# Optimization experiments

Measured on AMD Instinct MI355X. Metric: run time of the kernel, lower is better.

The kernel has to match this reference:

```python
import jax, jax.numpy as jnp
import numpy as np
import math


def setup_inputs() -> dict:
    key = jax.random.key(0)
    ks = jax.random.split(key, 4)
    B, C, H, W, D = 16, 512, 64, 64, 256
    return {
        "x": jax.random.normal(ks[0], (B, C, H, W), jnp.float32),
        "weight_global": jax.random.normal(ks[1], (C, D), jnp.float32) * 0.02,  # trunc_normal std=0.02
        "conv_g_w": jax.random.normal(ks[2], (C, C), jnp.float32) * 0.02,       # 1x1 conv, no bias
        "bn_g_gamma": jnp.ones((C,), jnp.float32),
        "bn_g_beta": jnp.zeros((C,), jnp.float32),
        "conv_c_w": jax.random.normal(ks[3], (C, C), jnp.float32) * 0.02,
        "bn_c_gamma": jnp.ones((C,), jnp.float32),
        "bn_c_beta": jnp.zeros((C,), jnp.float32),
    }


def _bn(x, gamma, beta, eps=1e-5):
    # BatchNorm2d in default training mode: batch statistics over (B, H, W)
    mean = x.mean(axis=(0, 2, 3), keepdims=True)
    var = x.var(axis=(0, 2, 3), keepdims=True)
    xn = (x - mean) * jax.lax.rsqrt(var + eps)
    return xn * gamma[None, :, None, None] + beta[None, :, None, None]


def reference(x, weight_global, conv_g_w, bn_g_gamma, bn_g_beta, conv_c_w, bn_c_gamma, bn_c_beta):
    b, c, h, w = x.shape
    inv_sqrt_c = 1.0 / math.sqrt(c)

    # Description: QR-orthogonal codebook, Q: (c, d)
    Q, _ = jnp.linalg.qr(weight_global + 1e-8)

    # global branch: 1x1 conv -> BN -> ReLU -> global avg pool
    gx = jnp.einsum('oc,bchw->bohw', conv_g_w, x)
    gx = jax.nn.relu(_bn(gx, bn_g_gamma, bn_g_beta))
    g = gx.mean(axis=(2, 3))                                  # (b, c)
    aff_g = jax.nn.softmax((g @ Q) * inv_sqrt_c, axis=1)      # (b, d)
    g = jax.nn.sigmoid(aff_g @ Q.T)                           # (b, c)

    # channel branch: 1x1 conv -> BN -> ReLU
    cx = jnp.einsum('oc,bchw->bohw', conv_c_w, x)
    cx = jax.nn.relu(_bn(cx, bn_c_gamma, bn_c_beta))
    ch = cx.reshape(b, c, h * w).transpose(0, 2, 1)           # (b, hw, c)
    aff_c = jax.nn.softmax((ch @ Q) * inv_sqrt_c, axis=2)     # (b, hw, d)
    # sum(diag_embed(aff_c) @ Q.T, dim=2) == aff_c @ Q.T (fused, avoids (b,hw,d,c) intermediate)
    ch = aff_c @ Q.T                                          # (b, hw, c)

    o = ch * g[:, None, :]
    o = o.transpose(0, 2, 1).reshape(b, c, h, w)
    return o + x
```

## Files before the change

### kernel.cpp

```cpp
#include <hip/hip_runtime.h>
#include <hip/hip_bf16.h>

#define BB 16
#define CC 512
#define HWP 4096
#define DD 256
#define NPIX 65536
#define INV_SQRT_C 0.04419417382415922f

typedef unsigned short u16;
typedef __attribute__((ext_vector_type(8))) short s16x8;
typedef __attribute__((ext_vector_type(8))) unsigned short u16x8;
typedef __attribute__((ext_vector_type(4))) unsigned short u16x4;
typedef __attribute__((ext_vector_type(4))) float f32x4;

__device__ __forceinline__ u16 f2b(float f){
  unsigned int u = __builtin_bit_cast(unsigned int, f);
  unsigned int r = (u + 0x7fffu + ((u >> 16) & 1u)) >> 16;
  return (u16)r;
}

__device__ __forceinline__ f32x4 mfma16(s16x8 a, s16x8 b, f32x4 c){
  return __builtin_amdgcn_mfma_f32_16x16x32_bf16(a, b, c, 0, 0, 0);
}

__global__ __launch_bounds__(512) void k_gram(const float* __restrict__ x, float* __restrict__ Spart,
                                              float* __restrict__ xbar, int kspl){
  __shared__ __align__(16) u16 Asl[128*72];
  __shared__ __align__(16) u16 Bsl[128*72];
  int tid = threadIdx.x;
  int w = tid >> 6, lane = tid & 63, lr = lane & 15, g = lane >> 4;
  int b = blockIdx.y;
  int kz = blockIdx.z;
  int t = blockIdx.x, ti = 0, rem = 4;
  while (t >= rem){ t -= rem; ++ti; --rem; }
  int tj = ti + t;
  int r0 = ti*128, c0 = tj*128;
  bool isdiag = (ti == tj);
  int wm = w >> 2, wn = w & 3;
  f32x4 acc[4][2] = {};
  float xsum[8] = {};
  const float* xb = x + (size_t)b*CC*HWP;
  int klen = HWP / kspl;
  int kbase = kz * klen;
  for (int k0 = kbase; k0 < kbase + klen; k0 += 64){
    __syncthreads();
    #pragma unroll
    for (int s = 0; s < 8; ++s){
      int tt = tid + s*512;
      int arr = tt >> 11;
      int row = (tt >> 4) & 127;
      int q = tt & 15;
      const float* src = xb + (size_t)((arr ? c0 : r0) + row)*HWP + k0 + q*4;
      f32x4 v = *(const f32x4*)src;
      if (isdiag && arr == 0) xsum[s] += (v[0]+v[1]) + (v[2]+v[3]);
      u16x4 u; u[0]=f2b(v[0]); u[1]=f2b(v[1]); u[2]=f2b(v[2]); u[3]=f2b(v[3]);
      u16* dst = (arr ? Bsl : Asl) + row*72 + q*4;
      *(u16x4*)dst = u;
    }
    __syncthreads();
    #pragma unroll
    for (int kc = 0; kc < 2; ++kc){
      s16x8 av[4], bv[2];
      #pragma unroll
      for (int mt = 0; mt < 4; ++mt) av[mt] = *(const s16x8*)&Asl[(wm*64 + mt*16 + lr)*72 + kc*32 + g*8];
      #pragma unroll
      for (int nt = 0; nt < 2; ++nt) bv[nt] = *(const s16x8*)&Bsl[(wn*32 + nt*16 + lr)*72 + kc*32 + g*8];
      #pragma unroll
      for (int mt = 0; mt < 4; ++mt)
        #pragma unroll
        for (int nt = 0; nt < 2; ++nt)
          acc[mt][nt] = mfma16(av[mt], bv[nt], acc[mt][nt]);
    }
  }
  float* sp = Spart + (size_t)(b*kspl + kz)*262144;
  #pragma unroll
  for (int mt = 0; mt < 4; ++mt)
    #pragma unroll
    for (int nt = 0; nt < 2; ++nt)
      #pragma unroll
      for (int r = 0; r < 4; ++r)
        sp[(size_t)(r0 + wm*64 + mt*16 + 4*g + r)*512 + c0 + wn*32 + nt*16 + lr] = acc[mt][nt][r];

  if (isdiag){
    __syncthreads();
    float* scr = (float*)Asl;
    #pragma unroll
    for (int s = 0; s < 8; ++s){
      int tt = tid + s*512;
      if ((tt >> 11) == 0){
        int row = (tt >> 4) & 127, q = tt & 15;
        scr[row*16 + q] = xsum[s];
      }
    }
    __syncthreads();
    if (tid < 128){
      float rs = 0.f;
      #pragma unroll
      for (int j = 0; j < 16; ++j) rs += scr[tid*16 + j];
      atomicAdd(&xbar[r0 + tid], rs * (1.0f/(float)NPIX));
    }
  }
}

__global__ __launch_bounds__(256) void k_sreduce(const float* __restrict__ Spart, float* __restrict__ S, int nslots){
  int idx = blockIdx.x*256 + threadIdx.x;
  int i = idx >> 9, j = idx & 511;
  int src = ((i >> 7) <= (j >> 7)) ? idx : (j*512 + i);
  float s = 0.f;
  for (int k = 0; k < nslots; ++k) s += Spart[(size_t)k*262144 + src];
  S[idx] = s;
}

__global__ __launch_bounds__(256) void k_G(const float* __restrict__ wg, float* __restrict__ G){
  int i = blockIdx.x, j = threadIdx.x;
  float s = 0.f;
  for (int c = 0; c < CC; ++c)
    s = fmaf(wg[c*DD + i] + 1e-8f, wg[c*DD + j] + 1e-8f, s);
  G[i*DD + j] = s;
}

__global__ __launch_bounds__(256) void k_cholPanel(float* __restrict__ G, int kb){
  int tid = threadIdx.x;
  int lane = tid & 63;
  int j = lane & 31;
  int K0 = kb*32;
  float c[32];
  #pragma unroll
  for (int i = 0; i < 32; ++i)
    c[i] = (i <= j) ? G[(K0+i)*DD + K0 + j] : 0.f;
  #pragma unroll
  for (int k = 0; k < 32; ++k){
    float piv = __shfl(c[k], k);
    float sd = sqrtf(piv);
    float ukj = c[k] / sd;
    c[k] = ukj;
    float uk[32];
    #pragma unroll
    for (int i = k + 1; i < 32; ++i) uk[i] = __shfl(ukj, i);
    #pragma unroll
    for (int i = k + 1; i < 32; ++i) c[i] -= uk[i] * ukj;
  }
  if (tid < 32){
    #pragma unroll
    for (int i = 0; i < 32; ++i)
      if (i <= j) G[(K0+i)*DD + K0 + j] = c[i];
  }
  int nt = 256 - K0 - 32;
  int jg = K0 + 32 + tid;
  if (tid < nt){
    float y[32];
    #pragma unroll
    for (int i = 0; i < 32; ++i) y[i] = G[(K0+i)*DD + jg];
    #pragma unroll
    for (int i = 0; i < 32; ++i){
      float s0 = y[i];
      #pragma unroll
      for (int l = 0; l < 32; ++l)
        if (l < i) s0 -= __shfl(c[l], i) * y[l];
      y[i] = s0 / __shfl(c[i], i);
    }
    #pragma unroll
    for (int i = 0; i < 32; ++i) G[(K0+i)*DD + jg] = y[i];
  }
}

__global__ __launch_bounds__(256) void k_cholTrail(float* __restrict__ G, int kb){
  int K0 = kb*32;
  int nt = 256 - K0 - 32;
  int T = (nt + 63) >> 6;
  int t = blockIdx.x, ti = 0, rem = T;
  while (t >= rem){ t -= rem; ++ti; --rem; }
  int tj = ti + t;
  int r0 = K0 + 32 + ti*64;
  int c0 = K0 + 32 + tj*64;
  __shared__ __align__(16) float Ur[32][64];
  __shared__ __align__(16) float Uc[32][64];
  int tid = threadIdx.x;
  for (int idx = tid; idx < 2048; idx += 256){
    int k = idx >> 6, cc = idx & 63;
    int gr = r0 + cc, gc = c0 + cc;
    Ur[k][cc] = (gr < 256) ? G[(K0+k)*DD + gr] : 0.f;
    Uc[k][cc] = (gc < 256) ? G[(K0+k)*DD + gc] : 0.f;
  }
  __syncthreads();
  int tr = (tid >> 4) * 4;
  int tc = (tid & 15) * 4;
  float acc[4][4] = {};
  #pragma unroll
  for (int k = 0; k < 32; ++k){
    f32x4 a = *(const f32x4*)&Ur[k][tr];
    f32x4 b = *(const f32x4*)&Uc[k][tc];
    #pragma unroll
    for (int ii = 0; ii < 4; ++ii)
      #pragma unroll
      for (int jj = 0; jj < 4; ++jj)
        acc[ii][jj] += a[ii]*b[jj];
  }
  #pragma unroll
  for (int ii = 0; ii < 4; ++ii){
    int gi = r0 + tr + ii;
    if (gi >= 256) continue;
    #pragma unroll
    for (int jj = 0; jj < 4; ++jj){
      int gj = c0 + tc + jj;
      if (gj < 256 && gj >= gi)
        G[gi*DD + gj] -= acc[ii][jj];
    }
  }
}

__global__ __launch_bounds__(256) void k_qsolve(const float* __restrict__ G,
    const float* __restrict__ wg,
    float* __restrict__ Q, float* __restrict__ Qst,
    u16* __restrict__ Qb, u16* __restrict__ Qstb){
  __shared__ __align__(16) float Pp[8192];
  __shared__ float Qlds[256*64];
  __shared__ float Wred[3*32*64];
  int tid = threadIdx.x;
  int w = tid >> 6, lane = tid & 63;
  int c = blockIdx.x*64 + lane;
  const float* arow = wg + (size_t)c*DD;

  for (int J = 0; J < 8; ++J){
    int J0 = J*32;
    int nrows8 = (J0 + 32)*8;
    for (int idx = tid; idx < nrows8; idx += 256){
      int row = idx >> 3, q = idx & 7;
      *(f32x4*)&Pp[row*32 + q*4] = *(const f32x4*)&G[row*256 + J0 + q*4];
    }
    __syncthreads();

    float W[32];
    if (w == 0){
      #pragma unroll
      for (int r = 0; r < 32; ++r) W[r] = arow[J0 + r] + 1e-8f;
    } else {
      #pragma unroll
      for (int r = 0; r < 32; ++r) W[r] = 0.f;
    }
    for (int M = w; M < J; M += 4){
      #pragma unroll 4
      for (int k = 0; k < 32; ++k){
        int row = M*32 + k;
        float qv = Qlds[row*64 + lane];
        const float* pr = &Pp[row*32];
        #pragma unroll
        for (int r4 = 0; r4 < 8; ++r4){
          f32x4 p = *(const f32x4*)&pr[r4*4];
          W[r4*4+0] -= qv*p[0];
          W[r4*4+1] -= qv*p[1];
          W[r4*4+2] -= qv*p[2];
          W[r4*4+3] -= qv*p[3];
        }
      }
    }
    if (w > 0){
      #pragma unroll
      for (int r = 0; r < 32; ++r) Wred[((w-1)*32 + r)*64 + lane] = W[r];
    }
    __syncthreads();

    if (w == 0){
      #pragma unroll
      for (int r = 0; r < 32; ++r)
        W[r] += Wred[r*64 + lane] + Wred[(32+r)*64 + lane] + Wred[(64+r)*64 + lane];
      #pragma unroll
      for (int i = 0; i < 32; ++i){
        float t = W[i];
        for (int l = 0; l < i; ++l) t -= W[l] * Pp[(J0 + l)*32 + i];
        W[i] = t / Pp[(J0 + i)*32 + i];
      }
      #pragma unroll
      for (int i = 0; i < 32; ++i) Qlds[(J0 + i)*64 + lane] = W[i];
      #pragma unroll
      for (int r4 = 0; r4 < 8; ++r4){
        f32x4 q4; u16x4 qb4;
        #pragma unroll
        for (int jj = 0; jj < 4; ++jj){ q4[jj] = W[r4*4+jj]; qb4[jj] = f2b(W[r4*4+jj]); }
        *(f32x4*)&Q[(size_t)c*DD + J0 + r4*4] = q4;
        *(u16x4*)&Qb[(size_t)c*DD + J0 + r4*4] = qb4;
      }
      #pragma unroll
      for (int i = 0; i < 32; ++i){
        float qs = W[i] * INV_SQRT_C;
        Qst[(size_t)(J0 + i)*CC + c] = qs;
        Qstb[(size_t)(J0 + i)*CC + c] = f2b(qs);
      }
    }
    __syncthreads();
  }
}

__global__ __launch_bounds__(256) void k_fold(const float* __restrict__ Wg, const float* __restrict__ Wc,
    const float* __restrict__ gamg, const float* __restrict__ betg,
    const float* __restrict__ gamc, const float* __restrict__ betc,
    const float* __restrict__ S, const float* __restrict__ xbar,
    float* __restrict__ Wgf, float* __restrict__ bgf,
    float* __restrict__ Wcf, float* __restrict__ bcf,
    u16* __restrict__ Wgb, u16* __restrict__ Wcb){
  int o = blockIdx.x & 511, br = blockIdx.x >> 9;
  int tid = threadIdx.x;
  int wv = tid >> 6, lane = tid & 63;
  const float* W = br ? Wc : Wg;
  __shared__ float wrow[512];
  __shared__ float red[256];
  __shared__ float yred[4];
  __shared__ float sc_s, bi_s;
  wrow[tid] = W[o*512 + tid]; wrow[tid+256] = W[o*512 + tid + 256];
  __syncthreads();

  float qp = 0.f;
  for (int c1 = wv; c1 < 512; c1 += 4){
    const float* srow = S + (size_t)c1*512;
    float y = 0.f;
    #pragma unroll
    for (int c8 = 0; c8 < 8; ++c8){
      int c2 = lane + c8*64;
      y = fmaf(srow[c2], wrow[c2], y);
    }
    y += __shfl_xor(y, 1);
    y += __shfl_xor(y, 2);
    y += __shfl_xor(y, 4);
    y += __shfl_xor(y, 8);
    y += __shfl_xor(y, 16);
    y += __shfl_xor(y, 32);
    qp = fmaf(wrow[c1], y, qp);
  }
  if (lane == 0) yred[wv] = qp;

  float mp = 0.f;
  for (int c = tid; c < 512; c += 256) mp = fmaf(wrow[c], xbar[c], mp);
  red[tid] = mp; __syncthreads();
  for (int st = 128; st; st >>= 1){
    if (tid < st) red[tid] += red[tid+st];
    __syncthreads();
  }
  if (tid == 0){
    float m = red[0];
    float E = (yred[0] + yred[1] + yred[2] + yred[3]) * (1.0f/(float)NPIX);
    float var = E - m*m;
    float rstd = rsqrtf(var + 1e-5f);
    float gma = br ? gamc[o] : gamg[o];
    float bta = br ? betc[o] : betg[o];
    sc_s = gma * rstd;
    bi_s = bta - gma * rstd * m;
  }
  __syncthreads();
  float* Wf = br ? Wcf : Wgf;
  float* bf = br ? bcf : bgf;
  u16* Wb  = br ? Wcb : Wgb;
  float w0 = sc_s * wrow[tid], w1 = sc_s * wrow[tid+256];
  Wf[o*512 + tid]     = w0;
  Wf[o*512 + tid+256] = w1;
  Wb[o*512 + tid]     = f2b(w0);
  Wb[o*512 + tid+256] = f2b(w1);
  if (tid == 0) bf[o] = bi_s;
}

__global__ __launch_bounds__(512) void k_gconv(const float* __restrict__ x,
    const u16* __restrict__ Wb, const float* __restrict__ bf, float* __restrict__ gpart){
  __shared__ __align__(16) u16 Xs[64*512];
  int tid = threadIdx.x;
  int w = tid >> 6, lane = tid & 63, lr = lane & 15, g = lane >> 4;
  int slab = blockIdx.x, b = blockIdx.y;
  int p0 = slab*64;

  {
    const float* xb = x + (size_t)b*CC*HWP + p0;
    int p = tid & 63;
    int c8 = (tid >> 6) * 8;
    float v[64];
    #pragma unroll
    for (int pass = 0; pass < 8; ++pass)
      #pragma unroll
      for (int i = 0; i < 8; ++i)
        v[pass*8 + i] = xb[(size_t)(c8 + pass*64 + i)*HWP + p];
    #pragma unroll
    for (int pass = 0; pass < 8; ++pass){
      u16x8 u;
      #pragma unroll
      for (int i = 0; i < 8; ++i) u[i] = f2b(v[pass*8 + i]);
      *(u16x8*)&Xs[p*512 + ((c8 + pass*64) ^ ((p & 7) << 3))] = u;
    }
  }
  __syncthreads();

  f32x4 acc[4][4] = {};
  for (int k = 0; k < 16; ++k){
    int c0 = k*32 + g*8;
    s16x8 bv[4];
    #pragma unroll
    for (int pt = 0; pt < 4; ++pt){
      int p = pt*16 + lr;
      bv[pt] = *(const s16x8*)&Xs[p*512 + (c0 ^ ((p & 7) << 3))];
    }
    #pragma unroll
    for (int i = 0; i < 4; ++i){
      int o0 = (w*4 + i)*16;
      s16x8 a = *(const s16x8*)(Wb + (size_t)(o0 + lr)*512 + c0);
      #pragma unroll
      for (int pt = 0; pt < 4; ++pt)
        acc[i][pt] = mfma16(a, bv[pt], acc[i][pt]);
    }
  }
  #pragma unroll
  for (int i = 0; i < 4; ++i){
    int o0 = (w*4 + i)*16;
    f32x4 bias4 = *(const f32x4*)(bf + o0 + 4*g);
    float s[4] = {0.f, 0.f, 0.f, 0.f};
    #pragma unroll
    for (int pt = 0; pt < 4; ++pt)
      #pragma unroll
      for (int r = 0; r < 4; ++r)
        s[r] += fmaxf(acc[i][pt][r] + bias4[r], 0.f);
    #pragma unroll
    for (int r = 0; r < 4; ++r){
      s[r] += __shfl_xor(s[r], 1);
      s[r] += __shfl_xor(s[r], 2);
      s[r] += __shfl_xor(s[r], 4);
      s[r] += __shfl_xor(s[r], 8);
    }
    if (lr == 0){
      f32x4 sv; sv[0]=s[0]; sv[1]=s[1]; sv[2]=s[2]; sv[3]=s[3];
      *(f32x4*)(gpart + (size_t)(b*64 + slab)*512 + o0 + 4*g) = sv;
    }
  }
}

__global__ __launch_bounds__(256) void k_gvec(const float* __restrict__ gpart, const float* __restrict__ Q,
    const float* __restrict__ Qst, float* __restrict__ gvec){
  int b = blockIdx.x, tid = threadIdx.x;
  __shared__ float g0[512];
  __shared__ float aff[256];
  __shared__ float red[256];
  for (int o = tid; o < 512; o += 256){
    float s = 0.f;
    for (int sl = 0; sl < 64; ++sl) s += gpart[(size_t)(b*64 + sl)*512 + o];
    g0[o] = s * (1.0f/4096.0f);
  }
  __syncthreads();
  float l = 0.f;
  { const float* qr = Qst + (size_t)tid*512;
    for (int c = 0; c < 512; ++c) l = fmaf(qr[c], g0[c], l); }
  red[tid] = l; __syncthreads();
  for (int st = 128; st; st >>= 1){ if (tid < st) red[tid] = fmaxf(red[tid], red[tid+st]); __syncthreads(); }
  float m = red[0]; __syncthreads();
  float e = expf(l - m);
  red[tid] = e; __syncthreads();
  for (int st = 128; st; st >>= 1){ if (tid < st) red[tid] += red[tid+st]; __syncthreads(); }
  float inv = 1.0f/red[0];
  aff[tid] = e * inv;
  __syncthreads();
  for (int o = tid; o < 512; o += 256){
    const float* qr = Q + (size_t)o*DD;
    float v = 0.f;
    for (int d = 0; d < DD; ++d) v = fmaf(aff[d], qr[d], v);
    gvec[b*512 + o] = 1.0f/(1.0f + expf(-v));
  }
}

__global__ __launch_bounds__(512) void k_fused(const float* __restrict__ x,
    const u16* __restrict__ Wcb, const float* __restrict__ bcf,
    const u16* __restrict__ Qstb, const u16* __restrict__ Qb,
    const float* __restrict__ gvec, float* __restrict__ out){
  __shared__ __align__(16) u16 Xs[64*512];
  __shared__ __align__(16) u16 Ts[64*512];
  float* Lsf = (float*)Xs;
  u16*   As  = Ts;
  int tid = threadIdx.x;
  int w = tid >> 6, lane = tid & 63, lr = lane & 15, g = lane >> 4;
  int b = blockIdx.y, p0 = blockIdx.x*64;

  float xr[64];
  {
    const float* xb = x + (size_t)b*CC*HWP + p0;
    int p = tid & 63;
    int c8 = (tid >> 6) * 8;
    float v[64];
    #pragma unroll
    for (int pass = 0; pass < 8; ++pass)
      #pragma unroll
      for (int i = 0; i < 8; ++i)
        v[pass*8 + i] = xb[(size_t)(c8 + pass*64 + i)*HWP + p];
    #pragma unroll
    for (int pass = 0; pass < 8; ++pass){
      u16x8 u;
      #pragma unroll
      for (int i = 0; i < 8; ++i) u[i] = f2b(v[pass*8 + i]);
      *(u16x8*)&Xs[p*512 + ((c8 + pass*64) ^ ((p & 7) << 3))] = u;
    }
    #pragma unroll
    for (int i = 0; i < 4; ++i)
      #pragma unroll
      for (int pt = 0; pt < 4; ++pt)
        #pragma unroll
        for (int r = 0; r < 4; ++r)
          xr[(i*4 + pt)*4 + r] =
            x[(size_t)(b*CC + (w*4 + i)*16 + 4*g + r)*HWP + p0 + pt*16 + lr];
  }
  __syncthreads();

  {
    f32x4 acc[4][4] = {};
    for (int k = 0; k < 16; ++k){
      int c0 = k*32 + g*8;
      s16x8 bv[4];
      #pragma unroll
      for (int pt = 0; pt < 4; ++pt){
        int p = pt*16 + lr;
        bv[pt] = *(const s16x8*)&Xs[p*512 + (c0 ^ ((p & 7) << 3))];
      }
      #pragma unroll
      for (int i = 0; i < 4; ++i){
        int o0 = (w*4 + i)*16;
        s16x8 a = *(const s16x8*)(Wcb + (size_t)(o0 + lr)*512 + c0);
        #pragma unroll
        for (int pt = 0; pt < 4; ++pt)
          acc[i][pt] = mfma16(a, bv[pt], acc[i][pt]);
      }
    }
    #pragma unroll
    for (int i = 0; i < 4; ++i){
      int o0 = (w*4 + i)*16;
      f32x4 bias4 = *(const f32x4*)(bcf + o0 + 4*g);
      #pragma unroll
      for (int pt = 0; pt < 4; ++pt){
        int p = pt*16 + lr;
        u16x4 u;
        #pragma unroll
        for (int r = 0; r < 4; ++r) u[r] = f2b(fmaxf(acc[i][pt][r] + bias4[r], 0.f));
        *(u16x4*)&Ts[p*512 + ((o0 + 4*g) ^ ((p & 7) << 3))] = u;
      }
    }
  }
  __syncthreads();

  {
    f32x4 acc[2][4] = {};
    for (int k = 0; k < 16; ++k){
      int o0 = k*32 + g*8;
      s16x8 bv[4];
      #pragma unroll
      for (int pt = 0; pt < 4; ++pt){
        int p = pt*16 + lr;
        bv[pt] = *(const s16x8*)&Ts[p*512 + (o0 ^ ((p & 7) << 3))];
      }
      #pragma unroll
      for (int i = 0; i < 2; ++i){
        int d0 = (w*2 + i)*16;
        s16x8 a = *(const s16x8*)(Qstb + (size_t)(d0 + lr)*512 + o0);
        #pragma unroll
        for (int pt = 0; pt < 4; ++pt)
          acc[i][pt] = mfma16(a, bv[pt], acc[i][pt]);
      }
    }
    #pragma unroll
    for (int i = 0; i < 2; ++i){
      int d0 = (w*2 + i)*16;
      #pragma unroll
      for (int pt = 0; pt < 4; ++pt){
        int p = pt*16 + lr;
        *(f32x4*)&Lsf[p*256 + ((d0 + 4*g) ^ ((p & 7) << 2))] = acc[i][pt];
      }
    }
  }
  __syncthreads();

  {
    int px = tid >> 3, sub = tid & 7;
    float* Lrow = Lsf + px*256;
    int sw2 = (px & 7) << 2, sw3 = (px & 7) << 3;
    float v[32];
    #pragma unroll
    for (int jj = 0; jj < 8; ++jj){
      int d0 = sub*32 + jj*4;
      f32x4 t = *(const f32x4*)&Lrow[d0 ^ sw2];
      v[jj*4+0] = t[0]; v[jj*4+1] = t[1]; v[jj*4+2] = t[2]; v[jj*4+3] = t[3];
    }
    float m = v[0];
    #pragma unroll
    for (int jj = 1; jj < 32; ++jj) m = fmaxf(m, v[jj]);
    m = fmaxf(m, __shfl_xor(m, 1));
    m = fmaxf(m, __shfl_xor(m, 2));
    m = fmaxf(m, __shfl_xor(m, 4));
    float s = 0.f;
    #pragma unroll
    for (int jj = 0; jj < 32; ++jj){ v[jj] = __expf(v[jj] - m); s += v[jj]; }
    s += __shfl_xor(s, 1);
    s += __shfl_xor(s, 2);
    s += __shfl_xor(s, 4);
    float inv = 1.0f/s;
    #pragma unroll
    for (int jj = 0; jj < 4; ++jj){
      int d0 = sub*32 + jj*8;
      u16x8 u;
      #pragma unroll
      for (int i = 0; i < 8; ++i) u[i] = f2b(v[jj*8+i] * inv);
      *(u16x8*)&As[px*256 + (d0 ^ sw3)] = u;
    }
  }
  __syncthreads();

  {
    f32x4 acc[4][4] = {};
    for (int k = 0; k < 8; ++k){
      int d0 = k*32 + g*8;
      s16x8 bv[4];
      #pragma unroll
      for (int pt = 0; pt < 4; ++pt){
        int p = pt*16 + lr;
        bv[pt] = *(const s16x8*)&As[p*256 + (d0 ^ ((p & 7) << 3))];
      }
      #pragma unroll
      for (int i = 0; i < 4; ++i){
        int o0 = (w*4 + i)*16;
        s16x8 a = *(const s16x8*)(Qb + (size_t)(o0 + lr)*256 + d0);
        #pragma unroll
        for (int pt = 0; pt < 4; ++pt)
          acc[i][pt] = mfma16(a, bv[pt], acc[i][pt]);
      }
    }
    #pragma unroll
    for (int i = 0; i < 4; ++i){
      int o0 = (w*4 + i)*16;
      f32x4 gg = *(const f32x4*)(gvec + b*512 + o0 + 4*g);
      #pragma unroll
      for (int pt = 0; pt < 4; ++pt){
        #pragma unroll
        for (int r = 0; r < 4; ++r){
          size_t idx = (size_t)(b*CC + o0 + 4*g + r)*HWP + p0 + pt*16 + lr;
          out[idx] = fmaf(acc[i][pt][r], gg[r], xr[(i*4 + pt)*4 + r]);
        }
      }
    }
  }
}

extern "C" void kernel_launch(void* const* d_in, const int* in_sizes, int n_in,
                              void* d_out, int out_size, void* d_ws, size_t ws_size,
                              hipStream_t stream) {
  const float* x    = (const float*)d_in[0];
  const float* wg   = (const float*)d_in[1];
  const float* Wg   = (const float*)d_in[2];
  const float* gamg = (const float*)d_in[3];
  const float* betg = (const float*)d_in[4];
  const float* Wc   = (const float*)d_in[5];
  const float* gamc = (const float*)d_in[6];
  const float* betc = (const float*)d_in[7];
  float* out = (float*)d_out;

  int kspl = 1;
  {
    size_t need2 = ((size_t)1320448 + 2*16*262144 + 524288 + 393216) * 4;
    if (ws_size >= need2) kspl = 2;
  }

  float* ws = (float*)d_ws;
  float* G     = ws + 0;
  float* Q     = ws + 131072;
  float* Qst   = ws + 262144;
  float* S     = ws + 393216;
  float* xbar  = ws + 655360;
  float* Wgf   = ws + 655872;
  float* bgf   = ws + 918016;
  float* Wcf   = ws + 918528;
  float* bcf   = ws + 1180672;
  float* gvec  = ws + 1181184;
  float* Spart = ws + 1320448;
  float* gpart = Spart + (size_t)kspl*16*262144;
  u16*   ub    = (u16*)(gpart + 524288);
  u16* Qb   = ub;
  u16* Qstb = ub + 131072;
  u16* Wgb  = ub + 262144;
  u16* Wcb  = ub + 524288;

  hipMemsetAsync(xbar, 0, 512*sizeof(float), stream);
  k_gram<<<dim3(10,16,kspl), 512, 0, stream>>>(x, Spart, xbar, kspl);
  k_sreduce<<<1024, 256, 0, stream>>>(Spart, S, 16*kspl);
  k_G<<<256, 256, 0, stream>>>(wg, G);
  for (int kb = 0; kb < 8; ++kb){
    k_cholPanel<<<1, 256, 0, stream>>>(G, kb);
    int nt = 256 - kb*32 - 32;
    if (nt > 0){
      int T = (nt + 63) >> 6;
      k_cholTrail<<<T*(T+1)/2, 256, 0, stream>>>(G, kb);
    }
  }
  k_qsolve<<<8, 256, 0, stream>>>(G, wg, Q, Qst, Qb, Qstb);
  k_fold<<<1024, 256, 0, stream>>>(Wg, Wc, gamg, betg, gamc, betc, S, xbar, Wgf, bgf, Wcf, bcf, Wgb, Wcb);
  k_gconv<<<dim3(64,16), 512, 0, stream>>>(x, Wgb, bgf, gpart);
  k_gvec<<<16, 256, 0, stream>>>(gpart, Q, Qst, gvec);
  k_fused<<<dim3(64,16), 512, 0, stream>>>(x, Wcb, bcf, Qstb, Qb, gvec, out);
}
```

Measured before the change: 826.7 us.

## Merge Cholesky panel and trailing update kernels, fuse small setup kernels

Combines the S reduction and Gram-matrix kernels into one launch. It also merges each Cholesky panel factorization with its trailing update, so every block redundantly factors the 32x32 diagonal tile and solves its own row and column panels, writing the factor to a separate U buffer. This cuts the launch count of the serial Cholesky chain roughly in half. It also drops the unused fp32 folded-weight writes in k_fold and raises the gram k-split to 4 when the workspace allows. In exchange it adds redundant panel work per block and more partial-sum traffic in the S reduction.

```diff
diff --git a/kernel.cpp b/kernel.cpp
--- a/kernel.cpp
+++ b/kernel.cpp
@@ -103,28 +103,39 @@
   }
 }
 
-__global__ __launch_bounds__(256) void k_sreduce(const float* __restrict__ Spart, float* __restrict__ S, int nslots){
-  int idx = blockIdx.x*256 + threadIdx.x;
-  int i = idx >> 9, j = idx & 511;
-  int src = ((i >> 7) <= (j >> 7)) ? idx : (j*512 + i);
-  float s = 0.f;
-  for (int k = 0; k < nslots; ++k) s += Spart[(size_t)k*262144 + src];
-  S[idx] = s;
-}
-
-__global__ __launch_bounds__(256) void k_G(const float* __restrict__ wg, float* __restrict__ G){
-  int i = blockIdx.x, j = threadIdx.x;
-  float s = 0.f;
-  for (int c = 0; c < CC; ++c)
-    s = fmaf(wg[c*DD + i] + 1e-8f, wg[c*DD + j] + 1e-8f, s);
-  G[i*DD + j] = s;
-}
-
-__global__ __launch_bounds__(256) void k_cholPanel(float* __restrict__ G, int kb){
+__global__ __launch_bounds__(256) void k_sredG(const float* __restrict__ Spart, float* __restrict__ S,
+                                               int nslots, const float* __restrict__ wg, float* __restrict__ G){
+  if (blockIdx.x < 1024){
+    int idx = blockIdx.x*256 + threadIdx.x;
+    int i = idx >> 9, j = idx & 511;
+    int src = ((i >> 7) <= (j >> 7)) ? idx : (j*512 + i);
+    float s = 0.f;
+    for (int k = 0; k < nslots; ++k) s += Spart[(size_t)k*262144 + src];
+    S[idx] = s;
+  } else {
+    int i = blockIdx.x - 1024, j = threadIdx.x;
+    float s = 0.f;
+    for (int c = 0; c < CC; ++c)
+      s = fmaf(wg[c*DD + i] + 1e-8f, wg[c*DD + j] + 1e-8f, s);
+    G[i*DD + j] = s;
+  }
+}
+
+__global__ __launch_bounds__(256) void k_cholStep(float* __restrict__ G, float* __restrict__ U, int kb){
+  __shared__ __align__(16) float Ur[32][64];
+  __shared__ __align__(16) float Uc[32][64];
   int tid = threadIdx.x;
   int lane = tid & 63;
   int j = lane & 31;
   int K0 = kb*32;
+  int nt = 256 - K0 - 32;
+  int T = (nt + 63) >> 6;
+  int t = blockIdx.x, ti = 0, rem = T;
+  while (nt > 0 && t >= rem){ t -= rem; ++ti; --rem; }
+  int tj = ti + t;
+  int r0 = K0 + 32 + ti*64;
+  int c0 = K0 + 32 + tj*64;
+
   float c[32];
   #pragma unroll
   for (int i = 0; i < 32; ++i)
@@ -141,17 +152,21 @@
     #pragma unroll
     for (int i = k + 1; i < 32; ++i) c[i] -= uk[i] * ukj;
   }
-  if (tid < 32){
+  if (blockIdx.x == 0 && tid < 32){
     #pragma unroll
     for (int i = 0; i < 32; ++i)
-      if (i <= j) G[(K0+i)*DD + K0 + j] = c[i];
-  }
-  int nt = 256 - K0 - 32;
-  int jg = K0 + 32 + tid;
-  if (tid < nt){
+      if (i <= j) U[(K0+i)*DD + K0 + j] = c[i];
+  }
+  if (nt <= 0) return;
+
+  if (tid < 128){
+    int half = tid >> 6;
+    int cc = tid & 63;
+    int gc = (half ? c0 : r0) + cc;
+    bool act = gc < 256;
     float y[32];
     #pragma unroll
-    for (int i = 0; i < 32; ++i) y[i] = G[(K0+i)*DD + jg];
+    for (int i = 0; i < 32; ++i) y[i] = act ? G[(K0+i)*DD + gc] : 0.f;
     #pragma unroll
     for (int i = 0; i < 32; ++i){
       float s0 = y[i];
@@ -160,30 +175,20 @@
         if (l < i) s0 -= __shfl(c[l], i) * y[l];
       y[i] = s0 / __shfl(c[i], i);
     }
-    #pragma unroll
-    for (int i = 0; i < 32; ++i) G[(K0+i)*DD + jg] = y[i];
-  }
-}
-
-__global__ __launch_bounds__(256) void k_cholTrail(float* __restrict__ G, int kb){
-  int K0 = kb*32;
-  int nt = 256 - K0 - 32;
-  int T = (nt + 63) >> 6;
-  int t = blockIdx.x, ti = 0, rem = T;
-  while (t >= rem){ t -= rem; ++ti; --rem; }
-  int tj = ti + t;
-  int r0 = K0 + 32 + ti*64;
-  int c0 = K0 + 32 + tj*64;
-  __shared__ __align__(16) float Ur[32][64];
-  __shared__ __align__(16) float Uc[32][64];
-  int tid = threadIdx.x;
-  for (int idx = tid; idx < 2048; idx += 256){
-    int k = idx >> 6, cc = idx & 63;
-    int gr = r0 + cc, gc = c0 + cc;
-    Ur[k][cc] = (gr < 256) ? G[(K0+k)*DD + gr] : 0.f;
-    Uc[k][cc] = (gc < 256) ? G[(K0+k)*DD + gc] : 0.f;
-  }
-  __syncthreads();
+    if (act){
+      #pragma unroll
+      for (int i = 0; i < 32; ++i) U[(K0+i)*DD + gc] = y[i];
+    }
+    if (half){
+      #pragma unroll
+      for (int i = 0; i < 32; ++i) Uc[i][cc] = act ? y[i] : 0.f;
+    } else {
+      #pragma unroll
+      for (int i = 0; i < 32; ++i) Ur[i][cc] = act ? y[i] : 0.f;
+    }
+  }
+  __syncthreads();
+
   int tr = (tid >> 4) * 4;
   int tc = (tid & 15) * 4;
   float acc[4][4] = {};
@@ -210,7 +215,7 @@
   }
 }
 
-__global__ __launch_bounds__(256) void k_qsolve(const float* __restrict__ G,
+__global__ __launch_bounds__(256) void k_qsolve(const float* __restrict__ U,
     const float* __restrict__ wg,
     float* __restrict__ Q, float* __restrict__ Qst,
     u16* __restrict__ Qb, u16* __restrict__ Qstb){
@@ -227,7 +232,7 @@
     int nrows8 = (J0 + 32)*8;
     for (int idx = tid; idx < nrows8; idx += 256){
       int row = idx >> 3, q = idx & 7;
-      *(f32x4*)&Pp[row*32 + q*4] = *(const f32x4*)&G[row*256 + J0 + q*4];
+      *(f32x4*)&Pp[row*32 + q*4] = *(const f32x4*)&U[row*256 + J0 + q*4];
     }
     __syncthreads();
 
@@ -296,8 +301,7 @@
     const float* __restrict__ gamg, const float* __restrict__ betg,
     const float* __restrict__ gamc, const float* __restrict__ betc,
     const float* __restrict__ S, const float* __restrict__ xbar,
-    float* __restrict__ Wgf, float* __restrict__ bgf,
-    float* __restrict__ Wcf, float* __restrict__ bcf,
+    float* __restrict__ bgf, float* __restrict__ bcf,
     u16* __restrict__ Wgb, u16* __restrict__ Wcb){
   int o = blockIdx.x & 511, br = blockIdx.x >> 9;
   int tid = threadIdx.x;
@@ -347,14 +351,10 @@
     bi_s = bta - gma * rstd * m;
   }
   __syncthreads();
-  float* Wf = br ? Wcf : Wgf;
   float* bf = br ? bcf : bgf;
   u16* Wb  = br ? Wcb : Wgb;
-  float w0 = sc_s * wrow[tid], w1 = sc_s * wrow[tid+256];
-  Wf[o*512 + tid]     = w0;
-  Wf[o*512 + tid+256] = w1;
-  Wb[o*512 + tid]     = f2b(w0);
-  Wb[o*512 + tid+256] = f2b(w1);
+  Wb[o*512 + tid]     = f2b(sc_s * wrow[tid]);
+  Wb[o*512 + tid+256] = f2b(sc_s * wrow[tid+256]);
   if (tid == 0) bf[o] = bi_s;
 }
 
@@ -652,19 +652,19 @@
 
   int kspl = 1;
   {
-    size_t need2 = ((size_t)1320448 + 2*16*262144 + 524288 + 393216) * 4;
-    if (ws_size >= need2) kspl = 2;
+    size_t base = (size_t)1320448 + 524288 + 393216;
+    if (ws_size >= (base + (size_t)4*16*262144) * 4) kspl = 4;
+    else if (ws_size >= (base + (size_t)2*16*262144) * 4) kspl = 2;
   }
 
   float* ws = (float*)d_ws;
   float* G     = ws + 0;
+  float* U     = ws + 65536;
   float* Q     = ws + 131072;
   float* Qst   = ws + 262144;
   float* S     = ws + 393216;
   float* xbar  = ws + 655360;
-  float* Wgf   = ws + 655872;
   float* bgf   = ws + 918016;
-  float* Wcf   = ws + 918528;
   float* bcf   = ws + 1180672;
   float* gvec  = ws + 1181184;
   float* Spart = ws + 1320448;
@@ -677,18 +677,15 @@
 
   hipMemsetAsync(xbar, 0, 512*sizeof(float), stream);
   k_gram<<<dim3(10,16,kspl), 512, 0, stream>>>(x, Spart, xbar, kspl);
-  k_sreduce<<<1024, 256, 0, stream>>>(Spart, S, 16*kspl);
-  k_G<<<256, 256, 0, stream>>>(wg, G);
+  k_sredG<<<1280, 256, 0, stream>>>(Spart, S, 16*kspl, wg, G);
   for (int kb = 0; kb < 8; ++kb){
-    k_cholPanel<<<1, 256, 0, stream>>>(G, kb);
     int nt = 256 - kb*32 - 32;
-    if (nt > 0){
-      int T = (nt + 63) >> 6;
-      k_cholTrail<<<T*(T+1)/2, 256, 0, stream>>>(G, kb);
-    }
-  }
-  k_qsolve<<<8, 256, 0, stream>>>(G, wg, Q, Qst, Qb, Qstb);
-  k_fold<<<1024, 256, 0, stream>>>(Wg, Wc, gamg, betg, gamc, betc, S, xbar, Wgf, bgf, Wcf, bcf, Wgb, Wcb);
+    int T = (nt + 63) >> 6;
+    int nblk = (nt > 0) ? T*(T+1)/2 : 1;
+    k_cholStep<<<nblk, 256, 0, stream>>>(G, U, kb);
+  }
+  k_qsolve<<<8, 256, 0, stream>>>(U, wg, Q, Qst, Qb, Qstb);
+  k_fold<<<1024, 256, 0, stream>>>(Wg, Wc, gamg, betg, gamc, betc, S, xbar, bgf, bcf, Wgb, Wcb);
   k_gconv<<<dim3(64,16), 512, 0, stream>>>(x, Wgb, bgf, gpart);
   k_gvec<<<16, 256, 0, stream>>>(gpart, Q, Qst, gvec);
   k_fused<<<dim3(64,16), 512, 0, stream>>>(x, Wcb, bcf, Qstb, Qb, gvec, out);
```

Result: no change. 836.6 us (+1.2%).
